# Kernel tuning notes

Measured on AMD Instinct MI355X. Metric: run time of the kernel, lower is better.

Reference implementation:

```python
import jax, jax.numpy as jnp
import numpy as np

S, B, H = 2048, 2, 4096
NH, NG, HD = 32, 8, 128  # heads, kv groups, head size


def setup_inputs() -> dict:
    key = jax.random.key(0)
    k1, k2, k3 = jax.random.split(key, 3)
    x = jax.random.normal(k1, (S, B, H), jnp.float32)
    qkv_h = H + 2 * HD * NG  # 6144
    W_qkv = jax.random.normal(k2, (qkv_h, H), jnp.float32) * 0.02
    b_qkv = jnp.zeros((qkv_h,), jnp.float32)
    W_dense = jax.random.normal(k3, (H, H), jnp.float32) * 0.02
    # rope cache: gen_rope_cache(S, n_elem=HD) -> [S, HD//2, 2] (cos, sin)
    theta = 1.0 / (10000.0 ** (jnp.arange(0, HD, 2, dtype=jnp.float32) / HD))
    ang = jnp.outer(jnp.arange(S, dtype=jnp.float32), theta)
    rope_cache = jnp.stack([jnp.cos(ang), jnp.sin(ang)], axis=-1)
    return {"x": x, "rope_cache": rope_cache, "W_qkv": W_qkv, "b_qkv": b_qkv, "W_dense": W_dense}


def _apply_rope(x, rope):
    # x: [S, B, nh, D]; rope: [S, D//2, 2]
    s, b, nh, d = x.shape
    half = rope.shape[1]
    rot = 2 * half
    xr = x[..., :rot].reshape(s, b, nh, half, 2)
    cos = rope[:s, None, None, :, 0]
    sin = rope[:s, None, None, :, 1]
    out = jnp.stack([xr[..., 0] * cos - xr[..., 1] * sin,
                     xr[..., 1] * cos + xr[..., 0] * sin], axis=-1)
    return jnp.concatenate([out.reshape(s, b, nh, rot), x[..., rot:]], axis=-1)


def reference(x, rope_cache, W_qkv, b_qkv, W_dense):
    s, b, h = x.shape
    qkv = x @ W_qkv.T + b_qkv  # [S, B, H + 2*NG*HD]
    q, k, v = jnp.split(qkv, [h, h + NG * HD], axis=-1)
    q = q.reshape(s, b, NH, HD)
    k = k.reshape(s, b, NG, HD)
    v = v.reshape(s, b, NG, HD)
    q = _apply_rope(q, rope_cache)
    k = _apply_rope(k, rope_cache)
    rep = NH // NG  # GQA expand: each kv group repeated contiguously (expand+view)
    k = jnp.repeat(k, rep, axis=2)
    v = jnp.repeat(v, rep, axis=2)
    q, k, v = (t.transpose(1, 2, 0, 3) for t in (q, k, v))  # [B, NH, S, HD]
    scale = 1.0 / jnp.sqrt(jnp.asarray(HD, x.dtype))
    scores = jnp.einsum('bhqd,bhkd->bhqk', q, k) * scale
    causal = jnp.tril(jnp.ones((s, s), bool))
    scores = jnp.where(causal, scores, jnp.finfo(scores.dtype).min)
    attn = jax.nn.softmax(scores, axis=-1)
    out = jnp.einsum('bhqk,bhkd->bhqd', attn, v)
    out = out.transpose(2, 0, 1, 3).reshape(s, b, h)  # [S, B, H]
    return out @ W_dense.T
```

## Files before the change

kernel.cpp:

```cpp
#include <hip/hip_runtime.h>
#include <hip/hip_bf16.h>
#include <cstdint>
#include <cstddef>

#define S_LEN   2048
#define BATCH   2
#define HDIM    4096
#define NHEADS  32
#define NGROUPS 8
#define HEADD   128
#define QKV_N   6144

typedef __attribute__((ext_vector_type(8))) short  short8;
typedef __attribute__((ext_vector_type(4))) float  floatx4;

__device__ __forceinline__ void async_ld16(const void* g, void* l) {
  __builtin_amdgcn_global_load_lds((const __attribute__((address_space(1))) void*)g,
                                   (__attribute__((address_space(3))) void*)l,
                                   16, 0, 0);
}

__device__ __forceinline__ unsigned short f2bf_bits(float f) {
  unsigned int u = __float_as_uint(f);
  u += 0x7FFFu + ((u >> 16) & 1u);
  return (unsigned short)(u >> 16);
}

__global__ void cvt_f32_bf16(const float4* __restrict__ in,
                             ushort4* __restrict__ out, int n4)
{
  const int i = blockIdx.x * blockDim.x + threadIdx.x;
  if (i >= n4) return;
  const float4 v = in[i];
  ushort4 o;
  o.x = f2bf_bits(v.x); o.y = f2bf_bits(v.y);
  o.z = f2bf_bits(v.z); o.w = f2bf_bits(v.w);
  out[i] = o;
}

template<int MODE>
__global__ void __launch_bounds__(512, 2)
gemm256(const __hip_bfloat16* __restrict__ A,
        const __hip_bfloat16* __restrict__ Bm,
        const float* __restrict__ bias,
        float* __restrict__ Cout,
        __hip_bfloat16* __restrict__ Qbuf,
        __hip_bfloat16* __restrict__ Kbuf,
        __hip_bfloat16* __restrict__ Vtbuf,
        int M, int N, int K)
{
  __shared__ __align__(16) short As[2][2][128*64];
  __shared__ __align__(16) short Bs[2][2][128*64];

  const int nbx = N >> 8;
  const int nwg = (M >> 8) * nbx;
  int bid = blockIdx.x;
  { const int cpx = nwg >> 3; bid = (bid & 7) * cpx + (bid >> 3); }
  const int mb = bid / nbx, nb = bid - mb * nbx;

  const int tid  = threadIdx.x;
  const int wave = tid >> 6, lane = tid & 63;
  const int wm = wave >> 2, wn = wave & 3;
  const int quad = lane >> 4, l15 = lane & 15;

  const __hip_bfloat16* Abase = A  + (size_t)mb * 256 * K;
  const __hip_bfloat16* Bbase = Bm + (size_t)nb * 256 * K;

  floatx4 acc[8][4] = {};
  short8  afr[4][2];
  short8  bfr[4][2];

#define BARRIER() do { __builtin_amdgcn_s_barrier(); \
                       asm volatile("" ::: "memory"); } while (0)

#define STAGE_A(buf, half, kb) do { \
    const __hip_bfloat16* src_ = Abase + (size_t)((half)*128) * K + (kb); \
    _Pragma("unroll") \
    for (int j_ = 0; j_ < 2; ++j_) { \
      const int cb_  = j_*512 + wave*64; \
      const int idx_ = cb_ + lane; \
      const int r_ = idx_ >> 3, gc_ = (idx_ & 7) ^ (r_ & 7); \
      async_ld16(src_ + (size_t)r_*K + gc_*8, &As[buf][half][cb_*8]); \
    } } while (0)

#define STAGE_B(buf, half, kb) do { \
    const __hip_bfloat16* src_ = Bbase + (size_t)((half)*128) * K + (kb); \
    _Pragma("unroll") \
    for (int j_ = 0; j_ < 2; ++j_) { \
      const int cb_  = j_*512 + wave*64; \
      const int idx_ = cb_ + lane; \
      const int r_ = idx_ >> 3, gc_ = (idx_ & 7) ^ (r_ & 7); \
      async_ld16(src_ + (size_t)r_*K + gc_*8, &Bs[buf][half][cb_*8]); \
    } } while (0)

#define LDA4(buf, mh) do { \
    _Pragma("unroll") \
    for (int mi_ = 0; mi_ < 4; ++mi_) { \
      const short* b_ = &As[buf][wm][(((mh)*4 + mi_)*16 + l15)*64]; \
      _Pragma("unroll") \
      for (int ks_ = 0; ks_ < 2; ++ks_) \
        afr[mi_][ks_] = *(const short8*)&b_[((ks_*4 + quad) ^ (l15 & 7))*8]; \
    } } while (0)

#define LDB2(buf, nh) do { \
    _Pragma("unroll") \
    for (int ni_ = 0; ni_ < 2; ++ni_) { \
      const short* b_ = &Bs[buf][wn >> 1][((wn & 1)*64 + ((nh)*2 + ni_)*16 + l15)*64]; \
      _Pragma("unroll") \
      for (int ks_ = 0; ks_ < 2; ++ks_) \
        bfr[(nh)*2 + ni_][ks_] = *(const short8*)&b_[((ks_*4 + quad) ^ (l15 & 7))*8]; \
    } } while (0)

#define MFMA16(mh, nh) do { \
    asm volatile("s_waitcnt lgkmcnt(0)" ::: "memory"); \
    __builtin_amdgcn_s_setprio(1); \
    _Pragma("unroll") \
    for (int mi_ = 0; mi_ < 4; ++mi_) \
      _Pragma("unroll") \
      for (int ni_ = 0; ni_ < 2; ++ni_) \
        _Pragma("unroll") \
        for (int ks_ = 0; ks_ < 2; ++ks_) \
          acc[(mh)*4 + mi_][(nh)*2 + ni_] = \
              __builtin_amdgcn_mfma_f32_16x16x32_bf16( \
                  afr[mi_][ks_], bfr[(nh)*2 + ni_][ks_], \
                  acc[(mh)*4 + mi_][(nh)*2 + ni_], 0, 0, 0); \
    __builtin_amdgcn_s_setprio(0); \
  } while (0)

  STAGE_B(0, 0, 0);  STAGE_B(0, 1, 0);
  STAGE_A(0, 0, 0);  STAGE_A(0, 1, 0);
  STAGE_B(1, 0, 64); STAGE_B(1, 1, 64);
  asm volatile("s_waitcnt vmcnt(4)" ::: "memory");
  BARRIER();

  const int NI = K >> 7;
  for (int i = 0; i < NI; ++i) {
    const int kb1 = (i << 7) + 64;
    int kb2 = (i << 7) + 128; if (kb2 > K - 64) kb2 = K - 64;
    int kb3 = (i << 7) + 192; if (kb3 > K - 64) kb3 = K - 64;

    LDA4(0, 0); LDB2(0, 0);
    STAGE_A(1, 0, kb1);
    asm volatile("s_waitcnt lgkmcnt(8)" ::: "memory");
    BARRIER();
    MFMA16(0, 0);
    BARRIER();
    LDB2(0, 1);
    STAGE_A(1, 1, kb1);
    BARRIER();
    MFMA16(0, 1);
    BARRIER();
    LDA4(0, 1);
    STAGE_B(0, 0, kb2);
    BARRIER();
    MFMA16(1, 1);
    BARRIER();
    STAGE_B(0, 1, kb2);
    BARRIER();
    MFMA16(1, 0);
    asm volatile("s_waitcnt vmcnt(4)" ::: "memory");
    BARRIER();
    LDA4(1, 0); LDB2(1, 0);
    STAGE_A(0, 0, kb2);
    asm volatile("s_waitcnt lgkmcnt(8)" ::: "memory");
    BARRIER();
    MFMA16(0, 0);
    BARRIER();
    LDB2(1, 1);
    STAGE_A(0, 1, kb2);
    BARRIER();
    MFMA16(0, 1);
    BARRIER();
    LDA4(1, 1);
    STAGE_B(1, 0, kb3);
    BARRIER();
    MFMA16(1, 1);
    BARRIER();
    STAGE_B(1, 1, kb3);
    BARRIER();
    MFMA16(1, 0);
    asm volatile("s_waitcnt vmcnt(4)" ::: "memory");
    BARRIER();
  }

#undef BARRIER
#undef STAGE_A
#undef STAGE_B
#undef LDA4
#undef LDB2
#undef MFMA16

  #pragma unroll
  for (int mi = 0; mi < 8; ++mi) {
    #pragma unroll
    for (int ni = 0; ni < 4; ++ni) {
      const int n = nb*256 + wn*64 + ni*16 + l15;
      float bv = 0.0f;
      if (MODE == 1) bv = bias[n];
      #pragma unroll
      for (int r = 0; r < 4; ++r) {
        const int m = mb*256 + wm*128 + mi*16 + quad*4 + r;
        const float v = acc[mi][ni][r] + bv;
        if (MODE == 0) {
          Cout[(size_t)m*N + n] = v;
        } else {
          const __hip_bfloat16 hv = __float2bfloat16(v);
          const int s  = m >> 1;
          const int bi = m & 1;
          if (n < HDIM) {
            const int hh = n >> 7, d = n & 127;
            Qbuf[(((size_t)bi*NHEADS + hh)*S_LEN + s)*HEADD + d] = hv;
          } else if (n < HDIM + NGROUPS*HEADD) {
            const int gg = (n - HDIM) >> 7, d = n & 127;
            Kbuf[(((size_t)bi*NGROUPS + gg)*S_LEN + s)*HEADD + d] = hv;
          } else {
            const int gg = (n - (HDIM + NGROUPS*HEADD)) >> 7, d = n & 127;
            Vtbuf[(((size_t)bi*NGROUPS + gg)*HEADD + d)*S_LEN + s] = hv;
          }
        }
      }
    }
  }
}

__global__ void rope_kernel(__hip_bfloat16* __restrict__ Qbuf,
                            __hip_bfloat16* __restrict__ Kbuf,
                            const float* __restrict__ rope)
{
  const int QP = BATCH*NHEADS*S_LEN*64;
  const int KP = BATCH*NGROUPS*S_LEN*64;
  int idx = blockIdx.x * blockDim.x + threadIdx.x;
  __hip_bfloat16* base;
  int p;
  float post;
  if (idx < QP)            { base = Qbuf; p = idx;      post = 0.12751744061558475f; }
  else if (idx < QP + KP)  { base = Kbuf; p = idx - QP; post = 1.0f; }
  else return;
  const int i    = p & 63;
  const int rest = p >> 6;
  const int s    = rest & (S_LEN - 1);
  const float c  = rope[s*128 + 2*i];
  const float sn = rope[s*128 + 2*i + 1];
  __hip_bfloat16* ptr = base + (size_t)rest*HEADD + 2*i;
  const float x0 = __bfloat162float(ptr[0]);
  const float x1 = __bfloat162float(ptr[1]);
  ptr[0] = __float2bfloat16((x0*c - x1*sn) * post);
  ptr[1] = __float2bfloat16((x1*c + x0*sn) * post);
}

__global__ void __launch_bounds__(256)
attn_kernel(const __hip_bfloat16* __restrict__ Qbuf,
            const __hip_bfloat16* __restrict__ Kbuf,
            const __hip_bfloat16* __restrict__ Vtbuf,
            __hip_bfloat16* __restrict__ Obuf)
{
  __shared__ __align__(16) short KtS[64*128];
  __shared__ __align__(16) short VtS[128*64];
  __shared__ __align__(16) short PtS[4][16*72];

  const int qb   = blockIdx.x * 64;
  const int bh   = blockIdx.y;
  const int b    = bh >> 5, h = bh & 31;
  const int g    = h >> 2;
  const int tid  = threadIdx.x;
  const int wave = tid >> 6, lane = tid & 63;
  const int quad = lane >> 4, l15 = lane & 15;
  const int qw   = qb + wave*16;

  const __hip_bfloat16* Qp = Qbuf  + ((size_t)bh*S_LEN + qw) * HEADD;
  const __hip_bfloat16* Kp = Kbuf  + ((size_t)(b*NGROUPS + g)*S_LEN) * HEADD;
  const __hip_bfloat16* Vp = Vtbuf + ((size_t)(b*NGROUPS + g)*HEADD) * S_LEN;

  short8 aq[4];
  #pragma unroll
  for (int dc = 0; dc < 4; ++dc)
    aq[dc] = *(const short8*)&Qp[(size_t)l15*HEADD + dc*32 + quad*8];

  floatx4 O[8] = {};
  float li[4] = {0.f, 0.f, 0.f, 0.f};

  const int ktend = qb + 64;
  for (int kt = 0; kt < ktend; kt += 64) {
    #pragma unroll
    for (int i = 0; i < 4; ++i) {
      const int cb  = (i*4 + wave) * 64;
      const int idx = cb + lane;
      {
        const int r = idx >> 4, cl = idx & 15;
        const int gc = cl ^ (r & 15);
        async_ld16(Kp + (size_t)(kt + r)*HEADD + gc*8, KtS + cb*8);
      }
      {
        const int r = idx >> 3, cl = idx & 7;
        const int gc = cl ^ (r & 7);
        async_ld16(Vp + (size_t)r*S_LEN + kt + gc*8, VtS + cb*8);
      }
    }
    __syncthreads();

    floatx4 s[4] = {};
    #pragma unroll
    for (int dc = 0; dc < 4; ++dc) {
      #pragma unroll
      for (int kc = 0; kc < 4; ++kc) {
        const int row = kc*16 + l15;
        const int ch  = (dc*4 + quad) ^ l15;
        const short8 bk = *(const short8*)&KtS[row*128 + ch*8];
        s[kc] = __builtin_amdgcn_mfma_f32_16x16x32_bf16(aq[dc], bk, s[kc], 0, 0, 0);
      }
    }

    if (kt == qb) {
      #pragma unroll
      for (int r = 0; r < 4; ++r) {
        const int row = qw + quad*4 + r;
        float rs = 0.f;
        #pragma unroll
        for (int kc = 0; kc < 4; ++kc) {
          const int col = kt + kc*16 + l15;
          const float p = (col > row) ? 0.0f : __builtin_amdgcn_exp2f(s[kc][r]);
          s[kc][r] = p; rs += p;
        }
        li[r] += rs;
      }
    } else {
      #pragma unroll
      for (int r = 0; r < 4; ++r) {
        float rs = 0.f;
        #pragma unroll
        for (int kc = 0; kc < 4; ++kc) {
          const float p = __builtin_amdgcn_exp2f(s[kc][r]);
          s[kc][r] = p; rs += p;
        }
        li[r] += rs;
      }
    }

    #pragma unroll
    for (int r = 0; r < 4; ++r)
      #pragma unroll
      for (int kc = 0; kc < 4; ++kc)
        PtS[wave][(quad*4 + r)*72 + kc*16 + l15] = (short)f2bf_bits(s[kc][r]);
    const short8 pa0 = *(const short8*)&PtS[wave][l15*72 +      quad*8];
    const short8 pa1 = *(const short8*)&PtS[wave][l15*72 + 32 + quad*8];

    #pragma unroll
    for (int dt = 0; dt < 8; ++dt) {
      const int row = dt*16 + l15;
      const int c0 = quad ^ (l15 & 7);
      const int c1 = (4 + quad) ^ (l15 & 7);
      const short8 bv0 = *(const short8*)&VtS[row*64 + c0*8];
      const short8 bv1 = *(const short8*)&VtS[row*64 + c1*8];
      O[dt] = __builtin_amdgcn_mfma_f32_16x16x32_bf16(pa0, bv0, O[dt], 0, 0, 0);
      O[dt] = __builtin_amdgcn_mfma_f32_16x16x32_bf16(pa1, bv1, O[dt], 0, 0, 0);
    }
    __syncthreads();
  }

  float inv[4];
  #pragma unroll
  for (int r = 0; r < 4; ++r) {
    float l = li[r];
    l += __shfl_xor(l, 1, 16);
    l += __shfl_xor(l, 2, 16);
    l += __shfl_xor(l, 4, 16);
    l += __shfl_xor(l, 8, 16);
    inv[r] = 1.0f / l;
  }
  #pragma unroll
  for (int dt = 0; dt < 8; ++dt)
    #pragma unroll
    for (int r = 0; r < 4; ++r) {
      const int row = qw + quad*4 + r;
      Obuf[((size_t)row*BATCH + b)*HDIM + h*HEADD + dt*16 + l15] =
          __float2bfloat16(O[dt][r] * inv[r]);
    }
}

extern "C" void kernel_launch(void* const* d_in, const int* in_sizes, int n_in,
                              void* d_out, int out_size, void* d_ws, size_t ws_size,
                              hipStream_t stream)
{
  const float* x    = (const float*)d_in[0];
  const float* rope = (const float*)d_in[1];
  const float* Wqkv = (const float*)d_in[2];
  const float* bqkv = (const float*)d_in[3];
  const float* Wd   = (const float*)d_in[4];
  float* out = (float*)d_out;

  const size_t MiB = 1024*1024;
  char* ws = (char*)d_ws;
  __hip_bfloat16* xb    = (__hip_bfloat16*)(ws);
  __hip_bfloat16* Wqkvb = (__hip_bfloat16*)(ws + 32*MiB);
  __hip_bfloat16* Wdb   = (__hip_bfloat16*)(ws + 80*MiB);
  __hip_bfloat16* Qbuf  = (__hip_bfloat16*)(ws + 112*MiB);
  __hip_bfloat16* Kbuf  = (__hip_bfloat16*)(ws + 144*MiB);
  __hip_bfloat16* Vt    = (__hip_bfloat16*)(ws + 152*MiB);
  __hip_bfloat16* Ob    = (__hip_bfloat16*)(ws + 160*MiB);

  {
    const int nx = S_LEN*BATCH*HDIM/4;
    const int nq = QKV_N*HDIM/4;
    const int nd = HDIM*HDIM/4;
    cvt_f32_bf16<<<(nx+255)/256, 256, 0, stream>>>((const float4*)x,    (ushort4*)xb,    nx);
    cvt_f32_bf16<<<(nq+255)/256, 256, 0, stream>>>((const float4*)Wqkv, (ushort4*)Wqkvb, nq);
    cvt_f32_bf16<<<(nd+255)/256, 256, 0, stream>>>((const float4*)Wd,   (ushort4*)Wdb,   nd);
  }

  gemm256<1><<<dim3((QKV_N/256)*((S_LEN*BATCH)/256)), dim3(512), 0, stream>>>(
      xb, Wqkvb, bqkv, nullptr, Qbuf, Kbuf, Vt, S_LEN*BATCH, QKV_N, HDIM);

  const int total_pairs = BATCH*(NHEADS+NGROUPS)*S_LEN*64;
  rope_kernel<<<total_pairs/256, 256, 0, stream>>>(Qbuf, Kbuf, rope);

  dim3 ga(S_LEN/64, BATCH*NHEADS);
  attn_kernel<<<ga, 256, 0, stream>>>(Qbuf, Kbuf, Vt, Ob);

  gemm256<0><<<dim3((HDIM/256)*((S_LEN*BATCH)/256)), dim3(512), 0, stream>>>(
      Ob, Wdb, nullptr, out, nullptr, nullptr, nullptr, S_LEN*BATCH, HDIM, HDIM);
}
```

Baseline: 895.9 us.

## Deepen GEMM prefetch pipeline, raise MFMA priority in attention, merge conversion kernels

The GEMM loads both K-halves of A and B into both buffers up front. It then reschedules the async global-to-LDS loads so the next-next tile is issued piecewise across the MFMA phases, gated by vmcnt(8) instead of vmcnt(4), which keeps more loads in flight. The attention kernel wraps its two MFMA loops in s_setprio(1) so matrix work is favoured over other waves. The three fp32-to-bf16 conversion launches become one launch with branch selection. The deeper prefetch reuses buffers more aggressively, so correctness rests on the waitcnt and barrier placement.

```diff
diff --git a/kernel.cpp b/kernel.cpp
--- a/kernel.cpp
+++ b/kernel.cpp
@@ -26,16 +26,25 @@
   return (unsigned short)(u >> 16);
 }
 
-__global__ void cvt_f32_bf16(const float4* __restrict__ in,
-                             ushort4* __restrict__ out, int n4)
+__global__ void cvt_all(const float4* __restrict__ x,
+                        const float4* __restrict__ wq,
+                        const float4* __restrict__ wd,
+                        ushort4* __restrict__ xo,
+                        ushort4* __restrict__ wqo,
+                        ushort4* __restrict__ wdo,
+                        int nx, int nq, int nd)
 {
-  const int i = blockIdx.x * blockDim.x + threadIdx.x;
-  if (i >= n4) return;
-  const float4 v = in[i];
+  int i = blockIdx.x * blockDim.x + threadIdx.x;
+  const float4* src; ushort4* dst; int off;
+  if (i < nx)                { src = x;  dst = xo;  off = i; }
+  else if (i < nx + nq)      { src = wq; dst = wqo; off = i - nx; }
+  else if (i < nx + nq + nd) { src = wd; dst = wdo; off = i - nx - nq; }
+  else return;
+  const float4 v = src[off];
   ushort4 o;
   o.x = f2bf_bits(v.x); o.y = f2bf_bits(v.y);
   o.z = f2bf_bits(v.z); o.w = f2bf_bits(v.w);
-  out[i] = o;
+  dst[off] = o;
 }
 
 template<int MODE>
@@ -72,25 +81,46 @@
 
 #define BARRIER() do { __builtin_amdgcn_s_barrier(); \
                        asm volatile("" ::: "memory"); } while (0)
-
-#define STAGE_A(buf, half, kb) do { \
-    const __hip_bfloat16* src_ = Abase + (size_t)((half)*128) * K + (kb); \
-    _Pragma("unroll") \
-    for (int j_ = 0; j_ < 2; ++j_) { \
-      const int cb_  = j_*512 + wave*64; \
+#define GATE(n)   asm volatile("s_waitcnt vmcnt(" #n ")" ::: "memory")
+
+#define SA_LO(buf, kb) do { \
+    _Pragma("unroll") \
+    for (int h_ = 0; h_ < 2; ++h_) { \
+      const int cb_  = wave*64; \
       const int idx_ = cb_ + lane; \
       const int r_ = idx_ >> 3, gc_ = (idx_ & 7) ^ (r_ & 7); \
-      async_ld16(src_ + (size_t)r_*K + gc_*8, &As[buf][half][cb_*8]); \
-    } } while (0)
-
-#define STAGE_B(buf, half, kb) do { \
-    const __hip_bfloat16* src_ = Bbase + (size_t)((half)*128) * K + (kb); \
-    _Pragma("unroll") \
-    for (int j_ = 0; j_ < 2; ++j_) { \
-      const int cb_  = j_*512 + wave*64; \
+      async_ld16(Abase + (size_t)(h_*128 + r_)*K + (kb) + gc_*8, \
+                 &As[buf][h_][cb_*8]); \
+    } } while (0)
+
+#define SA_HI(buf, kb) do { \
+    _Pragma("unroll") \
+    for (int h_ = 0; h_ < 2; ++h_) { \
+      const int cb_  = 512 + wave*64; \
       const int idx_ = cb_ + lane; \
       const int r_ = idx_ >> 3, gc_ = (idx_ & 7) ^ (r_ & 7); \
-      async_ld16(src_ + (size_t)r_*K + gc_*8, &Bs[buf][half][cb_*8]); \
+      async_ld16(Abase + (size_t)(h_*128 + r_)*K + (kb) + gc_*8, \
+                 &As[buf][h_][cb_*8]); \
+    } } while (0)
+
+#define SB_LO(buf, kb) do { \
+    _Pragma("unroll") \
+    for (int h_ = 0; h_ < 2; ++h_) { \
+      const int cb_  = wave*64; \
+      const int idx_ = cb_ + lane; \
+      const int r_ = idx_ >> 3, gc_ = (idx_ & 7) ^ (r_ & 7); \
+      async_ld16(Bbase + (size_t)(h_*128 + r_)*K + (kb) + gc_*8, \
+                 &Bs[buf][h_][cb_*8]); \
+    } } while (0)
+
+#define SB_HI(buf, kb) do { \
+    _Pragma("unroll") \
+    for (int h_ = 0; h_ < 2; ++h_) { \
+      const int cb_  = 512 + wave*64; \
+      const int idx_ = cb_ + lane; \
+      const int r_ = idx_ >> 3, gc_ = (idx_ & 7) ^ (r_ & 7); \
+      async_ld16(Bbase + (size_t)(h_*128 + r_)*K + (kb) + gc_*8, \
+                 &Bs[buf][h_][cb_*8]); \
     } } while (0)
 
 #define LDA4(buf, mh) do { \
@@ -127,65 +157,51 @@
     __builtin_amdgcn_s_setprio(0); \
   } while (0)
 
-  STAGE_B(0, 0, 0);  STAGE_B(0, 1, 0);
-  STAGE_A(0, 0, 0);  STAGE_A(0, 1, 0);
-  STAGE_B(1, 0, 64); STAGE_B(1, 1, 64);
-  asm volatile("s_waitcnt vmcnt(4)" ::: "memory");
+  SA_LO(0, 0);  SA_HI(0, 0);  SB_LO(0, 0);  SB_HI(0, 0);
+  SA_LO(1, 64); SA_HI(1, 64); SB_LO(1, 64); SB_HI(1, 64);
+  GATE(8);
   BARRIER();
 
   const int NI = K >> 7;
   for (int i = 0; i < NI; ++i) {
-    const int kb1 = (i << 7) + 64;
     int kb2 = (i << 7) + 128; if (kb2 > K - 64) kb2 = K - 64;
     int kb3 = (i << 7) + 192; if (kb3 > K - 64) kb3 = K - 64;
 
     LDA4(0, 0); LDB2(0, 0);
-    STAGE_A(1, 0, kb1);
     asm volatile("s_waitcnt lgkmcnt(8)" ::: "memory");
-    BARRIER();
-    MFMA16(0, 0);
-    BARRIER();
+    BARRIER(); MFMA16(0, 0); BARRIER();
     LDB2(0, 1);
-    STAGE_A(1, 1, kb1);
-    BARRIER();
-    MFMA16(0, 1);
-    BARRIER();
+    SA_LO(0, kb2);
+    BARRIER(); MFMA16(0, 1); BARRIER();
     LDA4(0, 1);
-    STAGE_B(0, 0, kb2);
-    BARRIER();
-    MFMA16(1, 1);
-    BARRIER();
-    STAGE_B(0, 1, kb2);
-    BARRIER();
-    MFMA16(1, 0);
-    asm volatile("s_waitcnt vmcnt(4)" ::: "memory");
+    SB_LO(0, kb2); SB_HI(0, kb2);
+    BARRIER(); MFMA16(1, 1); BARRIER();
+    SA_HI(0, kb2);
+    BARRIER(); MFMA16(1, 0);
+    GATE(8);
     BARRIER();
     LDA4(1, 0); LDB2(1, 0);
-    STAGE_A(0, 0, kb2);
     asm volatile("s_waitcnt lgkmcnt(8)" ::: "memory");
-    BARRIER();
-    MFMA16(0, 0);
-    BARRIER();
+    BARRIER(); MFMA16(0, 0); BARRIER();
     LDB2(1, 1);
-    STAGE_A(0, 1, kb2);
-    BARRIER();
-    MFMA16(0, 1);
-    BARRIER();
+    SA_LO(1, kb3);
+    BARRIER(); MFMA16(0, 1); BARRIER();
     LDA4(1, 1);
-    STAGE_B(1, 0, kb3);
-    BARRIER();
-    MFMA16(1, 1);
-    BARRIER();
-    STAGE_B(1, 1, kb3);
-    BARRIER();
-    MFMA16(1, 0);
-    asm volatile("s_waitcnt vmcnt(4)" ::: "memory");
+    SB_LO(1, kb3); SB_HI(1, kb3);
+    BARRIER(); MFMA16(1, 1); BARRIER();
+    SA_HI(1, kb3);
+    BARRIER(); MFMA16(1, 0);
+    GATE(8);
     BARRIER();
   }
+  GATE(0);
 
 #undef BARRIER
-#undef STAGE_A
-#undef STAGE_B
+#undef GATE
+#undef SA_LO
+#undef SA_HI
+#undef SB_LO
+#undef SB_HI
 #undef LDA4
 #undef LDB2
 #undef MFMA16
@@ -299,6 +315,7 @@
     __syncthreads();
 
     floatx4 s[4] = {};
+    __builtin_amdgcn_s_setprio(1);
     #pragma unroll
     for (int dc = 0; dc < 4; ++dc) {
       #pragma unroll
@@ -309,6 +326,7 @@
         s[kc] = __builtin_amdgcn_mfma_f32_16x16x32_bf16(aq[dc], bk, s[kc], 0, 0, 0);
       }
     }
+    __builtin_amdgcn_s_setprio(0);
 
     if (kt == qb) {
       #pragma unroll
@@ -344,6 +362,7 @@
     const short8 pa0 = *(const short8*)&PtS[wave][l15*72 +      quad*8];
     const short8 pa1 = *(const short8*)&PtS[wave][l15*72 + 32 + quad*8];
 
+    __builtin_amdgcn_s_setprio(1);
     #pragma unroll
     for (int dt = 0; dt < 8; ++dt) {
       const int row = dt*16 + l15;
@@ -354,6 +373,8 @@
       O[dt] = __builtin_amdgcn_mfma_f32_16x16x32_bf16(pa0, bv0, O[dt], 0, 0, 0);
       O[dt] = __builtin_amdgcn_mfma_f32_16x16x32_bf16(pa1, bv1, O[dt], 0, 0, 0);
     }
+    __builtin_amdgcn_s_setprio(0);
+
     __syncthreads();
   }
 
@@ -402,9 +423,10 @@
     const int nx = S_LEN*BATCH*HDIM/4;
     const int nq = QKV_N*HDIM/4;
     const int nd = HDIM*HDIM/4;
-    cvt_f32_bf16<<<(nx+255)/256, 256, 0, stream>>>((const float4*)x,    (ushort4*)xb,    nx);
-    cvt_f32_bf16<<<(nq+255)/256, 256, 0, stream>>>((const float4*)Wqkv, (ushort4*)Wqkvb, nq);
-    cvt_f32_bf16<<<(nd+255)/256, 256, 0, stream>>>((const float4*)Wd,   (ushort4*)Wdb,   nd);
+    const int nt = nx + nq + nd;
+    cvt_all<<<(nt+255)/256, 256, 0, stream>>>(
+        (const float4*)x, (const float4*)Wqkv, (const float4*)Wd,
+        (ushort4*)xb, (ushort4*)Wqkvb, (ushort4*)Wdb, nx, nq, nd);
   }
 
   gemm256<1><<<dim3((QKV_N/256)*((S_LEN*BATCH)/256)), dim3(512), 0, stream>>>(
```

Result: no change. 888.5 us (-0.8%).
